# Performance work log

Hardware: AMD Instinct MI355X
Metric: run time of the kernel (lower is better)

## Reference

```python
import jax, jax.numpy as jnp
import numpy as np

B, T, F, U = 8192, 21, 3, 512


def setup_inputs() -> dict:
    key = jax.random.key(0)
    ks = jax.random.split(key, 10)
    s = 0.05  # weight scale
    return {
        "x": jax.random.normal(ks[0], (B, T, F), jnp.float32),
        "learn_type_all": jax.random.randint(ks[1], (T, B), 0, 2).astype(jnp.int32),
        "kernel": jax.random.normal(ks[2], (F, 4 * U), jnp.float32) * s,
        "recurrent_kernel": jax.random.normal(ks[3], (U, 4 * U), jnp.float32) * s,
        "bias": jnp.zeros((4 * U,), jnp.float32),
        "w_rnn": jax.random.normal(ks[4], (U, U), jnp.float32) * s,
        "u_rnn": jax.random.normal(ks[5], (U, U), jnp.float32) * s,
        "b_rnn": jnp.zeros((U,), jnp.float32),
        "w_fc": jax.random.normal(ks[6], (U, 32), jnp.float32) * s,
        "b_fc": jnp.zeros((32,), jnp.float32),
        "w_out": jax.random.normal(ks[7], (32, 1), jnp.float32) * s,
        "b_out": jnp.zeros((1,), jnp.float32),
    }


def _forward(x, learn_type_all, kernel, recurrent_kernel, bias,
             w_rnn, u_rnn, b_rnn, w_fc, b_fc, w_out, b_out):
    # Per-timestep, per-batch-row learn mask; if a timestep has no learned row,
    # the original forces row 0 to learn.
    mask = learn_type_all == 1                      # [T, B]
    any_learn = jnp.any(mask, axis=1)               # [T]
    mask = mask.at[:, 0].set(mask[:, 0] | ~any_learn)

    # For each row i, the output gate o comes from the most recent learned row
    # j <= i (forward fill); leading unlearned rows take the FIRST learned row's o.
    pos = jnp.where(mask, jnp.arange(B)[None, :], -1)      # [T, B]
    last_idx = jax.lax.cummax(pos, axis=1)                 # [T, B]
    first = jnp.argmax(mask, axis=1)                       # [T]
    o_idx = jnp.where(last_idx < 0, first[:, None], last_idx)  # [T, B]

    xs = jnp.moveaxis(x, 1, 0)  # [T, B, F]

    def lstm_cell(carry, inp):
        h, c = carry
        x_t, m_t, idx_t = inp
        # fused gate compute (implementation=2 path of the original)
        z = x_t @ kernel + h @ recurrent_kernel + bias     # [B, 4U]
        zi, zf, zg, zo = jnp.split(z, 4, axis=1)
        i_g = jax.nn.sigmoid(zi)
        f_g = jax.nn.sigmoid(zf)
        g_g = jnp.tanh(zg)
        o_comp = jax.nn.sigmoid(zo)
        # learned rows update carry; unlearned rows keep c_tm1
        c_new = jnp.where(m_t[:, None], f_g * c + i_g * g_g, c)
        o = o_comp[idx_t]                                  # gather prev-learned o
        h_new = o * jnp.tanh(c_new)
        return (h_new, c_new), h_new

    init = (jnp.zeros((B, U), x.dtype), jnp.zeros((B, U), x.dtype))
    (_, _), hs = jax.lax.scan(lstm_cell, init, (xs, mask, o_idx))  # hs: [T, B, U]

    # SimpleRNN over the LSTM output sequence (dropout inactive at inference)
    def srnn_cell(h, x_t):
        h_new = jnp.tanh(x_t @ w_rnn + h @ u_rnn + b_rnn)
        return h_new, None

    h_last, _ = jax.lax.scan(srnn_cell, jnp.zeros((B, U), x.dtype), hs)

    out = (h_last @ w_fc + b_fc) @ w_out + b_out           # [B, 1]
    return out


def reference(x, learn_type_all, kernel, recurrent_kernel, bias,
              w_rnn, u_rnn, b_rnn, w_fc, b_fc, w_out, b_out):
    return _forward(x, learn_type_all, kernel, recurrent_kernel, bias,
                    w_rnn, u_rnn, b_rnn, w_fc, b_fc, w_out, b_out)
```

## Files before the change

kernel.cpp:

```cpp
#include <hip/hip_runtime.h>
#include <stdint.h>

#define B_ 8192
#define T_ 21
#define F_ 3
#define U_ 512

typedef _Float16 f16x8 __attribute__((ext_vector_type(8)));
typedef float f32x4 __attribute__((ext_vector_type(4)));

__device__ __forceinline__ float fsigmoid(float x) { return 1.0f / (1.0f + __expf(-x)); }
__device__ __forceinline__ float ftanh_(float x) {
  float t = __expf(-2.0f * fabsf(x));
  float r = (1.0f - t) / (1.0f + t);
  return x < 0.0f ? -r : r;
}

__device__ __forceinline__ void gl_lds16(const void* g, void* l) {
  __builtin_amdgcn_global_load_lds((__attribute__((address_space(1))) void*)g,
                                   (__attribute__((address_space(3))) void*)l, 16, 0, 0);
}

__global__ void prep_weights(const float* __restrict__ Wr, const float* __restrict__ wrnn,
                             const float* __restrict__ urnn, const float* __restrict__ kern,
                             const float* __restrict__ bias,
                             _Float16* __restrict__ WrT, _Float16* __restrict__ W2T,
                             float* __restrict__ Kp, float* __restrict__ bp) {
  size_t i = (size_t)blockIdx.x * 256 + threadIdx.x;
  if (i < (size_t)2048 * 512) {
    int p = (int)(i >> 9), k = (int)(i & 511);
    int orig = ((p >> 4) & 3) * 512 + ((p >> 6) << 4) + (p & 15);
    WrT[i] = (_Float16)Wr[(size_t)k * 2048 + orig];
  }
  if (i < (size_t)512 * 1024) {
    int n = (int)(i >> 10), k = (int)(i & 1023);
    float v = (k < 512) ? wrnn[(size_t)k * 512 + n] : urnn[(size_t)(k - 512) * 512 + n];
    W2T[i] = (_Float16)v;
  }
  if (i < 2048) {
    int p = (int)i;
    int orig = ((p >> 4) & 3) * 512 + ((p >> 6) << 4) + (p & 15);
    Kp[p] = kern[orig];
    Kp[2048 + p] = kern[2048 + orig];
    Kp[4096 + p] = kern[4096 + orig];
    bp[p] = bias[orig];
  }
}

__global__ void prep_wv(const float* __restrict__ wfc, const float* __restrict__ bfc,
                        const float* __restrict__ wout, const float* __restrict__ bout,
                        float* __restrict__ wv) {
  int u = blockIdx.x * 256 + threadIdx.x;
  if (u < 512) {
    float s = 0.0f;
    for (int k = 0; k < 32; ++k) s += wfc[u * 32 + k] * wout[k];
    wv[u] = s;
  }
  if (u == 0) {
    float s = 0.0f;
    for (int k = 0; k < 32; ++k) s += bfc[k] * wout[k];
    wv[512] = s + bout[0];
  }
}

__global__ void prep_mask(const int* __restrict__ lt, int* __restrict__ orow,
                          int* __restrict__ idxL, int* __restrict__ idxU,
                          int* __restrict__ Mpad) {
  const int t = blockIdx.x;
  const int tid = threadIdx.x;
  __shared__ int sh[1024];
  __shared__ int s_any, s_first;
  if (tid == 0) { s_any = 0; s_first = 0x7fffffff; }
  __syncthreads();
  const int base = tid * 8;
  const int* row = lt + (size_t)t * B_ + base;
  int bits = 0;
#pragma unroll
  for (int j = 0; j < 8; ++j) bits |= (row[j] == 1) << j;
  if (bits) atomicOr(&s_any, 1);
  __syncthreads();
  if (tid == 0 && !s_any) bits |= 1;
  if (bits) atomicMin(&s_first, base + __ffs(bits) - 1);
  int lmax = -1;
#pragma unroll
  for (int j = 0; j < 8; ++j)
    if ((bits >> j) & 1) lmax = base + j;
  sh[tid] = lmax;
  __syncthreads();
  for (int off = 1; off < 1024; off <<= 1) {
    int v = (tid >= off) ? sh[tid - off] : -1;
    __syncthreads();
    if (v > sh[tid]) sh[tid] = v;
    __syncthreads();
  }
  const int prefix = (tid > 0) ? sh[tid - 1] : -1;
  __syncthreads();
  const int cnt = __popc(bits);
  sh[tid] = cnt;
  __syncthreads();
  for (int off = 1; off < 1024; off <<= 1) {
    int v = (tid >= off) ? sh[tid - off] : 0;
    __syncthreads();
    sh[tid] += v;
    __syncthreads();
  }
  const int excl = sh[tid] - cnt;
  const int total = sh[1023];
  const int first = s_first;
  int run = prefix, posL = excl, posU = base - excl;
  int* orp = orow + (size_t)t * B_ + base;
  int* ixL = idxL + (size_t)t * B_;
  int* ixU = idxU + (size_t)t * B_;
#pragma unroll
  for (int j = 0; j < 8; ++j) {
    if ((bits >> j) & 1) { ixL[posL++] = base + j; run = base + j; }
    else                 { ixU[posU++] = base + j; }
    orp[j] = (run < 0) ? first : run;
  }
  const int padded = (total + 127) & ~127;
  if (tid < padded - total) ixL[total + tid] = -1;
  const int totU = B_ - total;
  for (int i = totU + tid; i < B_; i += 1024) ixU[i] = -1;
  if (tid == 0) Mpad[t] = padded;
}

template <int MODE>
__device__ __forceinline__ void gemm_body(
    _Float16 (*__restrict__ Ab)[4096], _Float16 (*__restrict__ Bb)[4096],
    const _Float16* __restrict__ A0, const _Float16* __restrict__ A1,
    const _Float16* __restrict__ Wt, const float* __restrict__ x,
    const float* __restrict__ Kp, const float* __restrict__ bp,
    _Float16* __restrict__ cbuf, _Float16* __restrict__ og,
    _Float16* __restrict__ hnew, const float* __restrict__ brnn,
    _Float16* __restrict__ rout, const int* __restrict__ idxL,
    int mBase, int nBase, int t) {
  constexpr int K = (MODE == 0) ? 512 : 1024;
  constexpr int NT = K / 32;
  const int tid = threadIdx.x;
  const int w = tid >> 6, l = tid & 63;
  const int wm = w >> 1, wn = w & 1;
  const int lr = l >> 2;
  const int kq = (((l & 3) ^ ((lr >> 1) & 3)) << 3);
  const int ch0 = w * 2, ch1 = w * 2 + 1;

  int ra0, ra1;
  if constexpr (MODE == 0) {
    int i0 = idxL[mBase + ch0 * 16 + lr];
    int i1 = idxL[mBase + ch1 * 16 + lr];
    ra0 = i0 < 0 ? 0 : i0;
    ra1 = i1 < 0 ? 0 : i1;
  } else {
    ra0 = mBase + ch0 * 16 + lr;
    ra1 = mBase + ch1 * 16 + lr;
  }

  auto STAGE = [&](int bb, int kt) {
    const int k0 = kt * 32;
    const _Float16* As = A0;
    int koff = k0;
    if constexpr (MODE == 1) {
      if (k0 >= 512) { As = A1; koff = k0 - 512; }
    }
    gl_lds16(As + (size_t)ra0 * 512 + koff + kq, (char*)Ab[bb] + ch0 * 1024);
    gl_lds16(As + (size_t)ra1 * 512 + koff + kq, (char*)Ab[bb] + ch1 * 1024);
    gl_lds16(Wt + (size_t)(nBase + ch0 * 16 + lr) * K + k0 + kq, (char*)Bb[bb] + ch0 * 1024);
    gl_lds16(Wt + (size_t)(nBase + ch1 * 16 + lr) * K + k0 + kq, (char*)Bb[bb] + ch1 * 1024);
  };

  f32x4 acc[4][4] = {};
  STAGE(0, 0);
  STAGE(1, 1);
  STAGE(2, 2);
  const int fm = l & 15, fk = l >> 4;
  const int fro = fm * 32 + ((fk ^ ((fm >> 1) & 3)) << 3);
  for (int kt = 0; kt < NT; ++kt) {
    if (kt < NT - 2) {
      asm volatile("s_waitcnt vmcnt(8)" ::: "memory");
    } else if (kt == NT - 2) {
      asm volatile("s_waitcnt vmcnt(4)" ::: "memory");
    } else {
      asm volatile("s_waitcnt vmcnt(0)" ::: "memory");
    }
    __builtin_amdgcn_s_barrier();
    __builtin_amdgcn_sched_barrier(0);
    const int bb = kt & 3;
    f16x8 af[4], bf[4];
#pragma unroll
    for (int m = 0; m < 4; ++m)
      af[m] = *(const f16x8*)&Ab[bb][(wm * 64 + m * 16) * 32 + fro];
#pragma unroll
    for (int n = 0; n < 4; ++n)
      bf[n] = *(const f16x8*)&Bb[bb][(wn * 64 + n * 16) * 32 + fro];
    __builtin_amdgcn_s_setprio(1);
#pragma unroll
    for (int m = 0; m < 4; ++m)
#pragma unroll
      for (int n = 0; n < 4; ++n)
        acc[m][n] = __builtin_amdgcn_mfma_f32_16x16x32_f16(af[m], bf[n], acc[m][n], 0, 0, 0);
    __builtin_amdgcn_s_setprio(0);
    __builtin_amdgcn_sched_barrier(0);
    if (kt + 3 < NT) STAGE((kt + 3) & 3, kt + 3);
    __builtin_amdgcn_s_barrier();
  }

  const int c_ = l & 15, rg = l >> 4;
  const int pB = nBase + wn * 64;
  if constexpr (MODE == 0) {
    const int u = (pB >> 6) * 16 + c_;
    float kf[4][3], bb4[4];
#pragma unroll
    for (int n = 0; n < 4; ++n) {
      int p = pB + n * 16 + c_;
      kf[n][0] = Kp[p]; kf[n][1] = Kp[2048 + p]; kf[n][2] = Kp[4096 + p];
      bb4[n] = bp[p];
    }
#pragma unroll
    for (int m = 0; m < 4; ++m) {
#pragma unroll
      for (int r = 0; r < 4; ++r) {
        int bi = idxL[mBase + wm * 64 + m * 16 + rg * 4 + r];
        if (bi < 0) continue;
        const float* xp = x + (size_t)bi * (T_ * F_) + t * F_;
        float x0 = xp[0], x1 = xp[1], x2 = xp[2];
        float zi = acc[m][0][r] + x0 * kf[0][0] + x1 * kf[0][1] + x2 * kf[0][2] + bb4[0];
        float zf = acc[m][1][r] + x0 * kf[1][0] + x1 * kf[1][1] + x2 * kf[1][2] + bb4[1];
        float zg = acc[m][2][r] + x0 * kf[2][0] + x1 * kf[2][1] + x2 * kf[2][2] + bb4[2];
        float zo = acc[m][3][r] + x0 * kf[3][0] + x1 * kf[3][1] + x2 * kf[3][2] + bb4[3];
        float ig = fsigmoid(zi), fg = fsigmoid(zf);
        float gg = ftanh_(zg), ogv = fsigmoid(zo);
        size_t ci = (size_t)bi * 512 + u;
        float cold = (float)cbuf[ci];
        float cnew = fg * cold + ig * gg;
        cbuf[ci] = (_Float16)cnew;
        og[ci] = (_Float16)ogv;
        hnew[ci] = (_Float16)(ogv * ftanh_(cnew));
      }
    }
  } else {
#pragma unroll
    for (int m = 0; m < 4; ++m)
#pragma unroll
      for (int n = 0; n < 4; ++n) {
        int uu = pB + n * 16 + c_;
        float bn = brnn[uu];
#pragma unroll
        for (int r = 0; r < 4; ++r) {
          int b = mBase + wm * 64 + m * 16 + rg * 4 + r;
          rout[(size_t)b * 512 + uu] = (_Float16)ftanh_(acc[m][n][r] + bn);
        }
      }
  }
}

__global__ __launch_bounds__(256, 2) void fused_step(
    const _Float16* __restrict__ hprev, _Float16* __restrict__ hnew,
    const _Float16* __restrict__ rin, _Float16* __restrict__ rot,
    const _Float16* __restrict__ WrT, const _Float16* __restrict__ W2T,
    const float* __restrict__ x, const float* __restrict__ Kp,
    const float* __restrict__ bp, _Float16* __restrict__ cbuf,
    _Float16* __restrict__ og, const float* __restrict__ brnn,
    const int* __restrict__ idxL, const int* __restrict__ MpadP,
    int t, int yRnn) {
  __shared__ __align__(16) _Float16 Ab[4][4096];
  __shared__ __align__(16) _Float16 Bb[4][4096];
  if ((int)blockIdx.y < yRnn) {
    gemm_body<1>(Ab, Bb, hprev, rin, W2T, nullptr, nullptr, nullptr, nullptr, nullptr,
                 nullptr, brnn, rot, nullptr, blockIdx.x * 128, blockIdx.y * 128, t);
  } else {
    if ((int)blockIdx.x * 128 >= *MpadP) return;
    gemm_body<0>(Ab, Bb, hprev, nullptr, WrT, x, Kp, bp, cbuf, og, hnew, nullptr,
                 nullptr, idxL, blockIdx.x * 128, ((int)blockIdx.y - yRnn) * 128, t);
  }
}

__global__ __launch_bounds__(256, 2) void rnn_tail(
    const _Float16* __restrict__ h, const _Float16* __restrict__ rin,
    const _Float16* __restrict__ W2T, const float* __restrict__ brnn,
    _Float16* __restrict__ rot) {
  __shared__ __align__(16) _Float16 Ab[4][4096];
  __shared__ __align__(16) _Float16 Bb[4][4096];
  gemm_body<1>(Ab, Bb, h, rin, W2T, nullptr, nullptr, nullptr, nullptr, nullptr,
               nullptr, brnn, rot, nullptr, blockIdx.x * 128, blockIdx.y * 128, 0);
}

__global__ void gather_h(const _Float16* __restrict__ og, const _Float16* __restrict__ cbuf,
                         const int* __restrict__ orow, const int* __restrict__ idxU,
                         _Float16* __restrict__ h) {
  int g = blockIdx.x * 256 + threadIdx.x;
  int b = idxU[g >> 6];
  if (b < 0) return;
  int u0 = (g & 63) << 3;
  int src = orow[b];
  f16x8 ov = *(const f16x8*)(og + (size_t)src * 512 + u0);
  f16x8 cv = *(const f16x8*)(cbuf + (size_t)b * 512 + u0);
  f16x8 hv;
#pragma unroll
  for (int j = 0; j < 8; ++j) hv[j] = (_Float16)((float)ov[j] * ftanh_((float)cv[j]));
  *(f16x8*)(h + (size_t)b * 512 + u0) = hv;
}

__global__ void final_fc(const _Float16* __restrict__ r, const float* __restrict__ wv,
                         float* __restrict__ out) {
  int gw = (blockIdx.x * 256 + threadIdx.x) >> 6;
  int l = threadIdx.x & 63;
  const _Float16* rr = r + (size_t)gw * 512;
  f16x8 rv = *(const f16x8*)(rr + l * 8);
  const float4* wp = (const float4*)(wv + l * 8);
  float4 w0 = wp[0], w1 = wp[1];
  float wf[8] = {w0.x, w0.y, w0.z, w0.w, w1.x, w1.y, w1.z, w1.w};
  float s = 0.0f;
#pragma unroll
  for (int j = 0; j < 8; ++j) s += (float)rv[j] * wf[j];
  for (int o = 32; o; o >>= 1) s += __shfl_down(s, o);
  if (l == 0) out[gw] = s + wv[512];
}

extern "C" void kernel_launch(void* const* d_in, const int* in_sizes, int n_in,
                              void* d_out, int out_size, void* d_ws, size_t ws_size,
                              hipStream_t stream) {
  const float* x    = (const float*)d_in[0];
  const int*   lt   = (const int*)d_in[1];
  const float* kern = (const float*)d_in[2];
  const float* Wr   = (const float*)d_in[3];
  const float* bias = (const float*)d_in[4];
  const float* wrnn = (const float*)d_in[5];
  const float* urnn = (const float*)d_in[6];
  const float* brnn = (const float*)d_in[7];
  const float* wfc  = (const float*)d_in[8];
  const float* bfc  = (const float*)d_in[9];
  const float* wout = (const float*)d_in[10];
  const float* bout = (const float*)d_in[11];

  char* ws = (char*)d_ws;
  size_t off = 0;
  auto alloc = [&](size_t bytes) {
    void* p = ws + off;
    off = (off + bytes + 255) & ~(size_t)255;
    return p;
  };
  int*      orow = (int*)alloc((size_t)T_ * B_ * 4);
  int*      idxL = (int*)alloc((size_t)T_ * B_ * 4);
  int*      idxU = (int*)alloc((size_t)T_ * B_ * 4);
  int*      Mpad = (int*)alloc(T_ * 4);
  _Float16* cbuf = (_Float16*)alloc((size_t)B_ * U_ * 2);
  _Float16* h0   = (_Float16*)alloc((size_t)B_ * U_ * 2);
  _Float16* h1   = (_Float16*)alloc((size_t)B_ * U_ * 2);
  _Float16* r0   = (_Float16*)alloc((size_t)B_ * U_ * 2);
  _Float16* r1   = (_Float16*)alloc((size_t)B_ * U_ * 2);
  _Float16* og   = (_Float16*)alloc((size_t)B_ * U_ * 2);
  _Float16* WrT  = (_Float16*)alloc((size_t)2048 * 512 * 2);
  _Float16* W2T  = (_Float16*)alloc((size_t)512 * 1024 * 2);
  float*    Kp   = (float*)alloc(3 * 2048 * 4);
  float*    bp   = (float*)alloc(2048 * 4);
  float*    wv   = (float*)alloc(516 * 4);

  hipMemsetAsync(cbuf, 0, (size_t)B_ * U_ * 2, stream);
  hipMemsetAsync(h0, 0, (size_t)B_ * U_ * 2, stream);
  hipMemsetAsync(r0, 0, (size_t)B_ * U_ * 2, stream);

  prep_weights<<<4096, 256, 0, stream>>>(Wr, wrnn, urnn, kern, bias, WrT, W2T, Kp, bp);
  prep_wv<<<2, 256, 0, stream>>>(wfc, bfc, wout, bout, wv);
  prep_mask<<<T_, 1024, 0, stream>>>(lt, orow, idxL, idxU, Mpad);

  _Float16* hbuf[2] = {h0, h1};
  _Float16* rin = r0;
  _Float16* rot = r1;
  fused_step<<<dim3(64, 16), 256, 0, stream>>>(h0, h1, nullptr, nullptr, WrT, W2T, x,
                                               Kp, bp, cbuf, og, brnn, idxL, Mpad, 0, 0);
  gather_h<<<2048, 256, 0, stream>>>(og, cbuf, orow, idxU, h1);
  for (int t = 1; t < T_; ++t) {
    _Float16* hp = hbuf[t & 1];
    _Float16* hn = hbuf[(t + 1) & 1];
    fused_step<<<dim3(64, 20), 256, 0, stream>>>(hp, hn, rin, rot, WrT, W2T, x, Kp, bp,
                                                 cbuf, og, brnn,
                                                 idxL + (size_t)t * B_, Mpad + t, t, 4);
    _Float16* tmp = rin; rin = rot; rot = tmp;
    gather_h<<<2048, 256, 0, stream>>>(og, cbuf, orow + (size_t)t * B_,
                                       idxU + (size_t)t * B_, hn);
  }
  rnn_tail<<<dim3(64, 4), 256, 0, stream>>>(hbuf[T_ & 1], rin, W2T, brnn, rot);
  final_fc<<<2048, 256, 0, stream>>>(rot, wv, (float*)d_out);
}
```

Baseline: 1.109 ms.

## Fuse unlearned-row h fill into LSTM epilogue and shrink LDS pipeline to three stages

Drops the separate gather_h kernel and the og buffer. The mask prep now records, for each learned row, how many following unlearned rows (and, for the first learned row, the leading rows) inherit its output gate, and the GEMM epilogue writes h for those rows directly. This removes one launch per timestep plus an og write and read. The LDS ring buffer also goes from four stages to three, with one barrier removed, and launch bounds are raised to 3 blocks per CU for occupancy. The trade-off is that epilogue work becomes serial per run length, so long runs of unlearned rows can unbalance threads.

```diff
diff --git a/kernel.cpp b/kernel.cpp
--- a/kernel.cpp
+++ b/kernel.cpp
@@ -63,8 +63,8 @@
   }
 }
 
-__global__ void prep_mask(const int* __restrict__ lt, int* __restrict__ orow,
-                          int* __restrict__ idxL, int* __restrict__ idxU,
+__global__ void prep_mask(const int* __restrict__ lt, int* __restrict__ idxL,
+                          int* __restrict__ runF, int* __restrict__ runB,
                           int* __restrict__ Mpad) {
   const int t = blockIdx.x;
   const int tid = threadIdx.x;
@@ -81,20 +81,6 @@
   __syncthreads();
   if (tid == 0 && !s_any) bits |= 1;
   if (bits) atomicMin(&s_first, base + __ffs(bits) - 1);
-  int lmax = -1;
-#pragma unroll
-  for (int j = 0; j < 8; ++j)
-    if ((bits >> j) & 1) lmax = base + j;
-  sh[tid] = lmax;
-  __syncthreads();
-  for (int off = 1; off < 1024; off <<= 1) {
-    int v = (tid >= off) ? sh[tid - off] : -1;
-    __syncthreads();
-    if (v > sh[tid]) sh[tid] = v;
-    __syncthreads();
-  }
-  const int prefix = (tid > 0) ? sh[tid - 1] : -1;
-  __syncthreads();
   const int cnt = __popc(bits);
   sh[tid] = cnt;
   __syncthreads();
@@ -106,34 +92,49 @@
   }
   const int excl = sh[tid] - cnt;
   const int total = sh[1023];
+  __syncthreads();
+  const int firstL = bits ? (base + __ffs(bits) - 1) : 0x7fffffff;
+  sh[tid] = firstL;
+  __syncthreads();
+  for (int off = 1; off < 1024; off <<= 1) {
+    int v = (tid + off < 1024) ? sh[tid + off] : 0x7fffffff;
+    __syncthreads();
+    if (v < sh[tid]) sh[tid] = v;
+    __syncthreads();
+  }
+  const int nxtOut = (tid < 1023) ? sh[tid + 1] : 0x7fffffff;
   const int first = s_first;
-  int run = prefix, posL = excl, posU = base - excl;
-  int* orp = orow + (size_t)t * B_ + base;
   int* ixL = idxL + (size_t)t * B_;
-  int* ixU = idxU + (size_t)t * B_;
-#pragma unroll
-  for (int j = 0; j < 8; ++j) {
-    if ((bits >> j) & 1) { ixL[posL++] = base + j; run = base + j; }
-    else                 { ixU[posU++] = base + j; }
-    orp[j] = (run < 0) ? first : run;
-  }
+  int* rF = runF + (size_t)t * B_;
+  int* rB = runB + (size_t)t * B_;
+  int pos = excl;
+#pragma unroll
+  for (int j = 0; j < 8; ++j)
+    if ((bits >> j) & 1) ixL[pos++] = base + j;
+  int nl = nxtOut;
+#pragma unroll
+  for (int j = 7; j >= 0; --j)
+    if ((bits >> j) & 1) {
+      int r0 = base + j;
+      rF[r0] = ((nl == 0x7fffffff) ? (B_ - 1) : (nl - 1)) - r0;
+      rB[r0] = (r0 == first) ? r0 : 0;
+      nl = r0;
+    }
   const int padded = (total + 127) & ~127;
   if (tid < padded - total) ixL[total + tid] = -1;
-  const int totU = B_ - total;
-  for (int i = totU + tid; i < B_; i += 1024) ixU[i] = -1;
   if (tid == 0) Mpad[t] = padded;
 }
 
 template <int MODE>
-__device__ __forceinline__ void gemm_body(
+__device__ __forceinline__ void gemm_tile(
     _Float16 (*__restrict__ Ab)[4096], _Float16 (*__restrict__ Bb)[4096],
     const _Float16* __restrict__ A0, const _Float16* __restrict__ A1,
     const _Float16* __restrict__ Wt, const float* __restrict__ x,
     const float* __restrict__ Kp, const float* __restrict__ bp,
-    _Float16* __restrict__ cbuf, _Float16* __restrict__ og,
-    _Float16* __restrict__ hnew, const float* __restrict__ brnn,
-    _Float16* __restrict__ rout, const int* __restrict__ idxL,
-    int mBase, int nBase, int t) {
+    _Float16* __restrict__ cbuf, _Float16* __restrict__ hnew,
+    const float* __restrict__ brnn, _Float16* __restrict__ rout,
+    const int* __restrict__ idxL, const int* __restrict__ rF,
+    const int* __restrict__ rB, int mBase, int nBase, int t) {
   constexpr int K = (MODE == 0) ? 512 : 1024;
   constexpr int NT = K / 32;
   const int tid = threadIdx.x;
@@ -170,20 +171,17 @@
   f32x4 acc[4][4] = {};
   STAGE(0, 0);
   STAGE(1, 1);
-  STAGE(2, 2);
   const int fm = l & 15, fk = l >> 4;
   const int fro = fm * 32 + ((fk ^ ((fm >> 1) & 3)) << 3);
   for (int kt = 0; kt < NT; ++kt) {
-    if (kt < NT - 2) {
-      asm volatile("s_waitcnt vmcnt(8)" ::: "memory");
-    } else if (kt == NT - 2) {
+    if (kt + 1 < NT) {
       asm volatile("s_waitcnt vmcnt(4)" ::: "memory");
     } else {
       asm volatile("s_waitcnt vmcnt(0)" ::: "memory");
     }
     __builtin_amdgcn_s_barrier();
     __builtin_amdgcn_sched_barrier(0);
-    const int bb = kt & 3;
+    const int bb = kt % 3;
     f16x8 af[4], bf[4];
 #pragma unroll
     for (int m = 0; m < 4; ++m)
@@ -199,8 +197,7 @@
         acc[m][n] = __builtin_amdgcn_mfma_f32_16x16x32_f16(af[m], bf[n], acc[m][n], 0, 0, 0);
     __builtin_amdgcn_s_setprio(0);
     __builtin_amdgcn_sched_barrier(0);
-    if (kt + 3 < NT) STAGE((kt + 3) & 3, kt + 3);
-    __builtin_amdgcn_s_barrier();
+    if (kt + 2 < NT) STAGE((kt + 2) % 3, kt + 2);
   }
 
   const int c_ = l & 15, rg = l >> 4;
@@ -232,8 +229,17 @@
         float cold = (float)cbuf[ci];
         float cnew = fg * cold + ig * gg;
         cbuf[ci] = (_Float16)cnew;
-        og[ci] = (_Float16)ogv;
         hnew[ci] = (_Float16)(ogv * ftanh_(cnew));
+        int nf = rF[bi];
+        for (int k2 = 1; k2 <= nf; ++k2) {
+          size_t c2 = ci + (size_t)k2 * 512;
+          hnew[c2] = (_Float16)(ogv * ftanh_((float)cbuf[c2]));
+        }
+        int nb = rB[bi];
+        for (int k2 = 1; k2 <= nb; ++k2) {
+          size_t c2 = ci - (size_t)k2 * 512;
+          hnew[c2] = (_Float16)(ogv * ftanh_((float)cbuf[c2]));
+        }
       }
     }
   } else {
@@ -252,59 +258,45 @@
   }
 }
 
-__global__ __launch_bounds__(256, 2) void fused_step(
+__global__ __launch_bounds__(256, 3) void fused_step(
     const _Float16* __restrict__ hprev, _Float16* __restrict__ hnew,
     const _Float16* __restrict__ rin, _Float16* __restrict__ rot,
     const _Float16* __restrict__ WrT, const _Float16* __restrict__ W2T,
     const float* __restrict__ x, const float* __restrict__ Kp,
     const float* __restrict__ bp, _Float16* __restrict__ cbuf,
-    _Float16* __restrict__ og, const float* __restrict__ brnn,
-    const int* __restrict__ idxL, const int* __restrict__ MpadP,
-    int t, int yRnn) {
-  __shared__ __align__(16) _Float16 Ab[4][4096];
-  __shared__ __align__(16) _Float16 Bb[4][4096];
+    const float* __restrict__ brnn, const int* __restrict__ idxL,
+    const int* __restrict__ rF, const int* __restrict__ rB,
+    const int* __restrict__ MpadP, int t, int yRnn) {
+  __shared__ __align__(16) _Float16 Ab[3][4096];
+  __shared__ __align__(16) _Float16 Bb[3][4096];
   if ((int)blockIdx.y < yRnn) {
-    gemm_body<1>(Ab, Bb, hprev, rin, W2T, nullptr, nullptr, nullptr, nullptr, nullptr,
-                 nullptr, brnn, rot, nullptr, blockIdx.x * 128, blockIdx.y * 128, t);
+    gemm_tile<1>(Ab, Bb, hprev, rin, W2T, nullptr, nullptr, nullptr, nullptr,
+                 nullptr, brnn, rot, nullptr, nullptr, nullptr,
+                 blockIdx.x * 128, blockIdx.y * 128, t);
   } else {
     if ((int)blockIdx.x * 128 >= *MpadP) return;
-    gemm_body<0>(Ab, Bb, hprev, nullptr, WrT, x, Kp, bp, cbuf, og, hnew, nullptr,
-                 nullptr, idxL, blockIdx.x * 128, ((int)blockIdx.y - yRnn) * 128, t);
-  }
-}
-
-__global__ __launch_bounds__(256, 2) void rnn_tail(
+    gemm_tile<0>(Ab, Bb, hprev, nullptr, WrT, x, Kp, bp, cbuf, hnew,
+                 nullptr, nullptr, idxL, rF, rB,
+                 blockIdx.x * 128, ((int)blockIdx.y - yRnn) * 128, t);
+  }
+}
+
+__global__ __launch_bounds__(256, 3) void rnn_tail(
     const _Float16* __restrict__ h, const _Float16* __restrict__ rin,
     const _Float16* __restrict__ W2T, const float* __restrict__ brnn,
     _Float16* __restrict__ rot) {
-  __shared__ __align__(16) _Float16 Ab[4][4096];
-  __shared__ __align__(16) _Float16 Bb[4][4096];
-  gemm_body<1>(Ab, Bb, h, rin, W2T, nullptr, nullptr, nullptr, nullptr, nullptr,
-               nullptr, brnn, rot, nullptr, blockIdx.x * 128, blockIdx.y * 128, 0);
-}
-
-__global__ void gather_h(const _Float16* __restrict__ og, const _Float16* __restrict__ cbuf,
-                         const int* __restrict__ orow, const int* __restrict__ idxU,
-                         _Float16* __restrict__ h) {
-  int g = blockIdx.x * 256 + threadIdx.x;
-  int b = idxU[g >> 6];
-  if (b < 0) return;
-  int u0 = (g & 63) << 3;
-  int src = orow[b];
-  f16x8 ov = *(const f16x8*)(og + (size_t)src * 512 + u0);
-  f16x8 cv = *(const f16x8*)(cbuf + (size_t)b * 512 + u0);
-  f16x8 hv;
-#pragma unroll
-  for (int j = 0; j < 8; ++j) hv[j] = (_Float16)((float)ov[j] * ftanh_((float)cv[j]));
-  *(f16x8*)(h + (size_t)b * 512 + u0) = hv;
+  __shared__ __align__(16) _Float16 Ab[3][4096];
+  __shared__ __align__(16) _Float16 Bb[3][4096];
+  gemm_tile<1>(Ab, Bb, h, rin, W2T, nullptr, nullptr, nullptr, nullptr,
+               nullptr, brnn, rot, nullptr, nullptr, nullptr,
+               blockIdx.x * 128, blockIdx.y * 128, 0);
 }
 
 __global__ void final_fc(const _Float16* __restrict__ r, const float* __restrict__ wv,
                          float* __restrict__ out) {
   int gw = (blockIdx.x * 256 + threadIdx.x) >> 6;
   int l = threadIdx.x & 63;
-  const _Float16* rr = r + (size_t)gw * 512;
-  f16x8 rv = *(const f16x8*)(rr + l * 8);
+  f16x8 rv = *(const f16x8*)(r + (size_t)gw * 512 + l * 8);
   const float4* wp = (const float4*)(wv + l * 8);
   float4 w0 = wp[0], w1 = wp[1];
   float wf[8] = {w0.x, w0.y, w0.z, w0.w, w1.x, w1.y, w1.z, w1.w};
@@ -338,16 +330,15 @@
     off = (off + bytes + 255) & ~(size_t)255;
     return p;
   };
-  int*      orow = (int*)alloc((size_t)T_ * B_ * 4);
   int*      idxL = (int*)alloc((size_t)T_ * B_ * 4);
-  int*      idxU = (int*)alloc((size_t)T_ * B_ * 4);
+  int*      runF = (int*)alloc((size_t)T_ * B_ * 4);
+  int*      runB = (int*)alloc((size_t)T_ * B_ * 4);
   int*      Mpad = (int*)alloc(T_ * 4);
   _Float16* cbuf = (_Float16*)alloc((size_t)B_ * U_ * 2);
   _Float16* h0   = (_Float16*)alloc((size_t)B_ * U_ * 2);
   _Float16* h1   = (_Float16*)alloc((size_t)B_ * U_ * 2);
   _Float16* r0   = (_Float16*)alloc((size_t)B_ * U_ * 2);
   _Float16* r1   = (_Float16*)alloc((size_t)B_ * U_ * 2);
-  _Float16* og   = (_Float16*)alloc((size_t)B_ * U_ * 2);
   _Float16* WrT  = (_Float16*)alloc((size_t)2048 * 512 * 2);
   _Float16* W2T  = (_Float16*)alloc((size_t)512 * 1024 * 2);
   float*    Kp   = (float*)alloc(3 * 2048 * 4);
@@ -360,23 +351,23 @@
 
   prep_weights<<<4096, 256, 0, stream>>>(Wr, wrnn, urnn, kern, bias, WrT, W2T, Kp, bp);
   prep_wv<<<2, 256, 0, stream>>>(wfc, bfc, wout, bout, wv);
-  prep_mask<<<T_, 1024, 0, stream>>>(lt, orow, idxL, idxU, Mpad);
+  prep_mask<<<T_, 1024, 0, stream>>>(lt, idxL, runF, runB, Mpad);
 
   _Float16* hbuf[2] = {h0, h1};
   _Float16* rin = r0;
   _Float16* rot = r1;
   fused_step<<<dim3(64, 16), 256, 0, stream>>>(h0, h1, nullptr, nullptr, WrT, W2T, x,
-                                               Kp, bp, cbuf, og, brnn, idxL, Mpad, 0, 0);
-  gather_h<<<2048, 256, 0, stream>>>(og, cbuf, orow, idxU, h1);
+                                               Kp, bp, cbuf, brnn, idxL, runF, runB,
+                                               Mpad, 0, 0);
   for (int t = 1; t < T_; ++t) {
     _Float16* hp = hbuf[t & 1];
     _Float16* hn = hbuf[(t + 1) & 1];
     fused_step<<<dim3(64, 20), 256, 0, stream>>>(hp, hn, rin, rot, WrT, W2T, x, Kp, bp,
-                                                 cbuf, og, brnn,
-                                                 idxL + (size_t)t * B_, Mpad + t, t, 4);
+                                                 cbuf, brnn, idxL + (size_t)t * B_,
+                                                 runF + (size_t)t * B_,
+                                                 runB + (size_t)t * B_,
+                                                 Mpad + t, t, 4);
     _Float16* tmp = rin; rin = rot; rot = tmp;
-    gather_h<<<2048, 256, 0, stream>>>(og, cbuf, orow + (size_t)t * B_,
-                                       idxU + (size_t)t * B_, hn);
   }
   rnn_tail<<<dim3(64, 4), 256, 0, stream>>>(hbuf[T_ & 1], rin, W2T, brnn, rot);
   final_fc<<<2048, 256, 0, stream>>>(rot, wv, (float*)d_out);
```

Measured after the change: 1.260 ms. +13.6%, slower.

## Narrow RNN tiles to 128x64 and use a triple-buffered pipeline for occupancy

Applied to the files above, without the earlier changes.

The SimpleRNN GEMM tile shrinks from 128x128 to 128x64, with each wave owning 32 rows and all four N fragments, so the grid doubles along N (yRnn 4->8, grid y 20->24). The LDS ring goes from 4 to 3 stages with prefetch distance 2, and the trailing barrier is removed. Launch bounds rise to 3 blocks per CU. The aim is more resident blocks and better load balance against the LSTM tiles, at the cost of less B-operand reuse per tile, a shallower prefetch, and possible register pressure under the tighter launch bound.

```diff
diff --git a/kernel.cpp b/kernel.cpp
--- a/kernel.cpp
+++ b/kernel.cpp
@@ -125,7 +125,7 @@
 }
 
 template <int MODE>
-__device__ __forceinline__ void gemm_body(
+__device__ __forceinline__ void gemm_tile(
     _Float16 (*__restrict__ Ab)[4096], _Float16 (*__restrict__ Bb)[4096],
     const _Float16* __restrict__ A0, const _Float16* __restrict__ A1,
     const _Float16* __restrict__ Wt, const float* __restrict__ x,
@@ -138,7 +138,6 @@
   constexpr int NT = K / 32;
   const int tid = threadIdx.x;
   const int w = tid >> 6, l = tid & 63;
-  const int wm = w >> 1, wn = w & 1;
   const int lr = l >> 2;
   const int kq = (((l & 3) ^ ((lr >> 1) & 3)) << 3);
   const int ch0 = w * 2, ch1 = w * 2 + 1;
@@ -163,49 +162,56 @@
     }
     gl_lds16(As + (size_t)ra0 * 512 + koff + kq, (char*)Ab[bb] + ch0 * 1024);
     gl_lds16(As + (size_t)ra1 * 512 + koff + kq, (char*)Ab[bb] + ch1 * 1024);
-    gl_lds16(Wt + (size_t)(nBase + ch0 * 16 + lr) * K + k0 + kq, (char*)Bb[bb] + ch0 * 1024);
-    gl_lds16(Wt + (size_t)(nBase + ch1 * 16 + lr) * K + k0 + kq, (char*)Bb[bb] + ch1 * 1024);
+    if constexpr (MODE == 0) {
+      gl_lds16(Wt + (size_t)(nBase + ch0 * 16 + lr) * K + k0 + kq, (char*)Bb[bb] + ch0 * 1024);
+      gl_lds16(Wt + (size_t)(nBase + ch1 * 16 + lr) * K + k0 + kq, (char*)Bb[bb] + ch1 * 1024);
+    } else {
+      gl_lds16(Wt + (size_t)(nBase + w * 16 + lr) * K + k0 + kq, (char*)Bb[bb] + w * 1024);
+    }
   };
 
-  f32x4 acc[4][4] = {};
+  constexpr int MR = (MODE == 0) ? 4 : 2;
+  constexpr int NR = 4;
+  f32x4 acc[MR][NR] = {};
   STAGE(0, 0);
   STAGE(1, 1);
-  STAGE(2, 2);
   const int fm = l & 15, fk = l >> 4;
   const int fro = fm * 32 + ((fk ^ ((fm >> 1) & 3)) << 3);
+  const int wm = (MODE == 0) ? (w >> 1) : w;
+  const int wn = (MODE == 0) ? (w & 1) : 0;
   for (int kt = 0; kt < NT; ++kt) {
-    if (kt < NT - 2) {
-      asm volatile("s_waitcnt vmcnt(8)" ::: "memory");
-    } else if (kt == NT - 2) {
-      asm volatile("s_waitcnt vmcnt(4)" ::: "memory");
+    if (kt + 1 < NT) {
+      if constexpr (MODE == 0)
+        asm volatile("s_waitcnt vmcnt(4)" ::: "memory");
+      else
+        asm volatile("s_waitcnt vmcnt(3)" ::: "memory");
     } else {
       asm volatile("s_waitcnt vmcnt(0)" ::: "memory");
     }
     __builtin_amdgcn_s_barrier();
     __builtin_amdgcn_sched_barrier(0);
-    const int bb = kt & 3;
-    f16x8 af[4], bf[4];
-#pragma unroll
-    for (int m = 0; m < 4; ++m)
-      af[m] = *(const f16x8*)&Ab[bb][(wm * 64 + m * 16) * 32 + fro];
-#pragma unroll
-    for (int n = 0; n < 4; ++n)
-      bf[n] = *(const f16x8*)&Bb[bb][(wn * 64 + n * 16) * 32 + fro];
+    const int bb = kt % 3;
+    f16x8 af[MR], bf[NR];
+#pragma unroll
+    for (int m = 0; m < MR; ++m)
+      af[m] = *(const f16x8*)&Ab[bb][((MODE == 0 ? wm * 64 : w * 32) + m * 16) * 32 + fro];
+#pragma unroll
+    for (int n = 0; n < NR; ++n)
+      bf[n] = *(const f16x8*)&Bb[bb][((MODE == 0 ? wn * 64 : 0) + n * 16) * 32 + fro];
     __builtin_amdgcn_s_setprio(1);
 #pragma unroll
-    for (int m = 0; m < 4; ++m)
-#pragma unroll
-      for (int n = 0; n < 4; ++n)
+    for (int m = 0; m < MR; ++m)
+#pragma unroll
+      for (int n = 0; n < NR; ++n)
         acc[m][n] = __builtin_amdgcn_mfma_f32_16x16x32_f16(af[m], bf[n], acc[m][n], 0, 0, 0);
     __builtin_amdgcn_s_setprio(0);
     __builtin_amdgcn_sched_barrier(0);
-    if (kt + 3 < NT) STAGE((kt + 3) & 3, kt + 3);
-    __builtin_amdgcn_s_barrier();
+    if (kt + 2 < NT) STAGE((kt + 2) % 3, kt + 2);
   }
 
   const int c_ = l & 15, rg = l >> 4;
-  const int pB = nBase + wn * 64;
   if constexpr (MODE == 0) {
+    const int pB = nBase + wn * 64;
     const int u = (pB >> 6) * 16 + c_;
     float kf[4][3], bb4[4];
 #pragma unroll
@@ -238,21 +244,21 @@
     }
   } else {
 #pragma unroll
-    for (int m = 0; m < 4; ++m)
+    for (int m = 0; m < 2; ++m)
 #pragma unroll
       for (int n = 0; n < 4; ++n) {
-        int uu = pB + n * 16 + c_;
+        int uu = nBase + n * 16 + c_;
         float bn = brnn[uu];
 #pragma unroll
         for (int r = 0; r < 4; ++r) {
-          int b = mBase + wm * 64 + m * 16 + rg * 4 + r;
+          int b = mBase + w * 32 + m * 16 + rg * 4 + r;
           rout[(size_t)b * 512 + uu] = (_Float16)ftanh_(acc[m][n][r] + bn);
         }
       }
   }
 }
 
-__global__ __launch_bounds__(256, 2) void fused_step(
+__global__ __launch_bounds__(256, 3) void fused_step(
     const _Float16* __restrict__ hprev, _Float16* __restrict__ hnew,
     const _Float16* __restrict__ rin, _Float16* __restrict__ rot,
     const _Float16* __restrict__ WrT, const _Float16* __restrict__ W2T,
@@ -261,26 +267,29 @@
     _Float16* __restrict__ og, const float* __restrict__ brnn,
     const int* __restrict__ idxL, const int* __restrict__ MpadP,
     int t, int yRnn) {
-  __shared__ __align__(16) _Float16 Ab[4][4096];
-  __shared__ __align__(16) _Float16 Bb[4][4096];
+  __shared__ __align__(16) _Float16 Ab[3][4096];
+  __shared__ __align__(16) _Float16 Bb[3][4096];
   if ((int)blockIdx.y < yRnn) {
-    gemm_body<1>(Ab, Bb, hprev, rin, W2T, nullptr, nullptr, nullptr, nullptr, nullptr,
-                 nullptr, brnn, rot, nullptr, blockIdx.x * 128, blockIdx.y * 128, t);
+    gemm_tile<1>(Ab, Bb, hprev, rin, W2T, nullptr, nullptr, nullptr, nullptr,
+                 nullptr, nullptr, brnn, rot, nullptr,
+                 blockIdx.x * 128, blockIdx.y * 64, t);
   } else {
     if ((int)blockIdx.x * 128 >= *MpadP) return;
-    gemm_body<0>(Ab, Bb, hprev, nullptr, WrT, x, Kp, bp, cbuf, og, hnew, nullptr,
-                 nullptr, idxL, blockIdx.x * 128, ((int)blockIdx.y - yRnn) * 128, t);
-  }
-}
-
-__global__ __launch_bounds__(256, 2) void rnn_tail(
+    gemm_tile<0>(Ab, Bb, hprev, nullptr, WrT, x, Kp, bp, cbuf, og, hnew,
+                 nullptr, nullptr, idxL,
+                 blockIdx.x * 128, ((int)blockIdx.y - yRnn) * 128, t);
+  }
+}
+
+__global__ __launch_bounds__(256, 3) void rnn_tail(
     const _Float16* __restrict__ h, const _Float16* __restrict__ rin,
     const _Float16* __restrict__ W2T, const float* __restrict__ brnn,
     _Float16* __restrict__ rot) {
-  __shared__ __align__(16) _Float16 Ab[4][4096];
-  __shared__ __align__(16) _Float16 Bb[4][4096];
-  gemm_body<1>(Ab, Bb, h, rin, W2T, nullptr, nullptr, nullptr, nullptr, nullptr,
-               nullptr, brnn, rot, nullptr, blockIdx.x * 128, blockIdx.y * 128, 0);
+  __shared__ __align__(16) _Float16 Ab[3][4096];
+  __shared__ __align__(16) _Float16 Bb[3][4096];
+  gemm_tile<1>(Ab, Bb, h, rin, W2T, nullptr, nullptr, nullptr, nullptr,
+               nullptr, nullptr, brnn, rot, nullptr,
+               blockIdx.x * 128, blockIdx.y * 64, 0);
 }
 
 __global__ void gather_h(const _Float16* __restrict__ og, const _Float16* __restrict__ cbuf,
@@ -303,8 +312,7 @@
                          float* __restrict__ out) {
   int gw = (blockIdx.x * 256 + threadIdx.x) >> 6;
   int l = threadIdx.x & 63;
-  const _Float16* rr = r + (size_t)gw * 512;
-  f16x8 rv = *(const f16x8*)(rr + l * 8);
+  f16x8 rv = *(const f16x8*)(r + (size_t)gw * 512 + l * 8);
   const float4* wp = (const float4*)(wv + l * 8);
   float4 w0 = wp[0], w1 = wp[1];
   float wf[8] = {w0.x, w0.y, w0.z, w0.w, w1.x, w1.y, w1.z, w1.w};
@@ -371,13 +379,13 @@
   for (int t = 1; t < T_; ++t) {
     _Float16* hp = hbuf[t & 1];
     _Float16* hn = hbuf[(t + 1) & 1];
-    fused_step<<<dim3(64, 20), 256, 0, stream>>>(hp, hn, rin, rot, WrT, W2T, x, Kp, bp,
+    fused_step<<<dim3(64, 24), 256, 0, stream>>>(hp, hn, rin, rot, WrT, W2T, x, Kp, bp,
                                                  cbuf, og, brnn,
-                                                 idxL + (size_t)t * B_, Mpad + t, t, 4);
+                                                 idxL + (size_t)t * B_, Mpad + t, t, 8);
     _Float16* tmp = rin; rin = rot; rot = tmp;
     gather_h<<<2048, 256, 0, stream>>>(og, cbuf, orow + (size_t)t * B_,
                                        idxU + (size_t)t * B_, hn);
   }
-  rnn_tail<<<dim3(64, 4), 256, 0, stream>>>(hbuf[T_ & 1], rin, W2T, brnn, rot);
+  rnn_tail<<<dim3(64, 8), 256, 0, stream>>>(hbuf[T_ & 1], rin, W2T, brnn, rot);
   final_fc<<<2048, 256, 0, stream>>>(rot, wv, (float*)d_out);
 }
```

After: 1.032 ms. -7.0%, faster.
